# Kernel tuning notes

Hardware: AMD Instinct MI355X
Metric: run time of the kernel (lower is better)

## Reference

```python
import jax, jax.numpy as jnp
import numpy as np

EPS = 1e-06
K = 10
N, M, D, C = 65536, 1024, 2, 3


def setup_inputs() -> dict:
    key = jax.random.key(0)
    k1, k2, k3, k4 = jax.random.split(key, 4)
    x = jax.random.uniform(k1, (N, D), dtype=jnp.float32)            # query points (pixels)
    mus = jax.random.uniform(k2, (1, M, D), dtype=jnp.float32)        # gaussian means
    A = 0.1 * jax.random.normal(k3, (1, M, D, D), dtype=jnp.float32)  # random factor
    covs = A @ jnp.swapaxes(A, -1, -2) + 0.01 * jnp.eye(D, dtype=jnp.float32)  # SPD covariances
    cols = jax.random.uniform(k4, (1, M, C), dtype=jnp.float32)       # per-gaussian RGB
    return {"x": x, "mus": mus, "covs": covs, "cols": cols}


def reference(x, mus, covs, cols):
    # d: [N, M, D] point-to-mean offsets
    d = x[:, None, :] - mus[0]
    # solve covs @ s = d for each (point, gaussian) pair -> [N, M, D]
    s = jnp.linalg.solve(covs[0], d[..., None])[..., 0]
    # quadratic form d^T Sigma^{-1} d -> gaussian weights [N, M]
    gauss = jnp.exp(-0.5 * jnp.einsum('nmd,nmd->nm', d, s))
    k = min(K, mus.shape[1])
    vals, idx = jax.lax.top_k(gauss, k)              # [N, k]
    top_cols = cols[0][idx]                           # [N, k, C]
    raw = jnp.einsum('nk,nkc->nc', vals, top_cols)    # weighted color sum
    return raw / (vals.sum(-1, keepdims=True) + EPS)  # normalized [N, C]
```

## Files before the change

### kernel.cpp

```cpp
#include <hip/hip_runtime.h>
#include <stdint.h>

#define MG 1024
#define KTOP 10
#define EPSF 1e-6f
#define CXc 24
#define CYc 16
#define NCELL (CXc * CYc)
#define CAP 224
#define OVCAP 256
#define RHO 0.03757f
#define CSTRIDE 1040
#define CPAD 16
#define POISON 0xAAAAAAAAu

typedef unsigned long long u64;
typedef unsigned short u16;

__device__ __forceinline__ int cell_of(float x0, float x1) {
    int ix = (int)(x0 * CXc); ix = ix < 0 ? 0 : (ix > CXc - 1 ? CXc - 1 : ix);
    int iy = (int)(x1 * CYc); iy = iy < 0 ? 0 : (iy > CYc - 1 ? CYc - 1 : iy);
    return iy * CXc + ix;
}

__global__ __launch_bounds__(256) void k_prep(
    const float* __restrict__ x, const float* __restrict__ mus,
    const float* __restrict__ covs,
    uint32_t* __restrict__ counts, uint32_t* __restrict__ ovc,
    u16* __restrict__ ovlist, u16* __restrict__ buckets,
    float4* __restrict__ grec, float* __restrict__ grecC,
    u16* __restrict__ candM, uint32_t* __restrict__ ncand, int N)
{
    const int t = threadIdx.x, blk = blockIdx.x;
    if (blk < 256) {
        const int n = blk * 256 + t;
        if (n < MG) {
            const float4 cv = ((const float4*)covs)[n];
            const float2 mu = ((const float2*)mus)[n];
            const float inv = 1.0f / (cv.x * cv.w - cv.y * cv.z);
            grec[n]  = make_float4(mu.x, mu.y, -0.5f * cv.w * inv, cv.y * inv);
            grecC[n] = -0.5f * cv.x * inv;
        }
        if (n >= N) return;
        const float2 xv = ((const float2*)x)[n];
        const int c = cell_of(xv.x, xv.y);
        const uint32_t r = atomicAdd(&counts[c * CPAD], 1u) - POISON;
        if (r < CAP) buckets[c * CAP + r] = (u16)n;
        else { const uint32_t o = atomicAdd(ovc, 1u) - POISON; if (o < OVCAP) ovlist[o] = (u16)n; }
        return;
    }
    const int lane = t & 63;
    const int c = (blk - 256) * 4 + (t >> 6);
    const float cx = ((float)(c % CXc) + 0.5f) / (float)CXc;
    const float cy = ((float)(c / CXc) + 0.5f) / (float)CYc;
    const float INF = __builtin_huge_valf();

    float D10[KTOP], Uv[16];
    #pragma unroll
    for (int i = 0; i < KTOP; ++i) D10[i] = -INF;

    #pragma unroll
    for (int j = 0; j < 16; ++j) {
        const int m = j * 64 + lane;
        const float4 cv = ((const float4*)covs)[m];
        const float2 mu = ((const float2*)mus)[m];
        const float inv = 1.0f / (cv.x * cv.w - cv.y * cv.z);
        const float A = -0.5f * cv.w * inv, B = cv.y * inv, Cc = -0.5f * cv.x * inv;
        const float dx = cx - mu.x, dy = cy - mu.y;
        const float qc = fmaf(fmaf(A, dx, B * dy), dx, Cc * (dy * dy));
        const float S00 = -2.0f * A, S01 = -B, S11 = -2.0f * Cc;
        const float sx = S00 * dx + S01 * dy, sy = S01 * dx + S11 * dy;
        const float slack = sqrtf(fmaf(sx, sx, sy * sy)) * RHO;
        const float lr2 = 0.5f * (S00 + S11) * (RHO * RHO);
        const float eps = 1e-3f * (1.0f + fabsf(qc) + slack);
        Uv[j] = qc + slack + eps;
        const float D = qc - slack - lr2 - eps;
        bool cg[KTOP];
        #pragma unroll
        for (int i = 0; i < KTOP; ++i) cg[i] = D10[i] >= D;
        #pragma unroll
        for (int i = KTOP - 1; i >= 1; --i)
            D10[i] = cg[i] ? D10[i] : (cg[i - 1] ? D : D10[i - 1]);
        D10[0] = cg[0] ? D10[0] : D;
    }
    #pragma unroll
    for (int s = 1; s < 64; s <<= 1) {
        float ob[KTOP], na[KTOP];
        #pragma unroll
        for (int i = 0; i < KTOP; ++i) ob[i] = __shfl_xor(D10[i], s);
        #pragma unroll
        for (int i = 0; i < KTOP; ++i) {
            float best = -INF;
            #pragma unroll
            for (int j = 0; j <= i + 1 && j <= KTOP; ++j) {
                const int l = i + 1 - j;
                if (l > KTOP) continue;
                const float av = (j == 0) ? INF : D10[j - 1];
                const float bv = (l == 0) ? INF : ob[l - 1];
                best = fmaxf(best, fminf(av, bv));
            }
            na[i] = best;
        }
        #pragma unroll
        for (int i = 0; i < KTOP; ++i) D10[i] = na[i];
    }
    const float L = D10[KTOP - 1];

    const int base = c * CSTRIDE;
    const u64 below = (lane == 0) ? 0ull : ((~0ull) >> (64 - lane));
    int total = 0;
    #pragma unroll
    for (int j = 0; j < 16; ++j) {
        const bool keep = (Uv[j] >= L);
        const u64 bal = __ballot(keep);
        if (keep) {
            const int slot = total + (int)__popcll(bal & below);
            candM[base + slot] = (u16)(j * 64 + lane);
        }
        total += (int)__popcll(bal);
    }
    if (lane == 0) ncand[c] = (uint32_t)total;
}

__global__ __launch_bounds__(128) void k_main(
    const float* __restrict__ x, const float* __restrict__ cols,
    const float4* __restrict__ grec, const float* __restrict__ grecC,
    const uint32_t* __restrict__ counts, const uint32_t* __restrict__ ovc,
    const u16* __restrict__ ovlist, const u16* __restrict__ buckets,
    const u16* __restrict__ candM, const uint32_t* __restrict__ ncand,
    float* __restrict__ out, int N)
{
    __shared__ float4 l4[CSTRIDE];
    __shared__ __align__(16) float lC[CSTRIDE];
    __shared__ __align__(16) uint32_t lM[CSTRIDE];

    const int t = threadIdx.x;
    const int lane = t & 63, wv = t >> 6;
    const int b = blockIdx.x;

    u64 topk[KTOP];
    const u64 SENT = ((u64)0x007FFFFFull) << 10;
    #pragma unroll
    for (int j = 0; j < KTOP; ++j) topk[j] = SENT;
    float thr = __uint_as_float(0xff800000u);

    auto net_insert = [&](u64 key) {
        bool cg[KTOP];
        #pragma unroll
        for (int j = 0; j < KTOP; ++j) cg[j] = topk[j] >= key;
        #pragma unroll
        for (int j = KTOP - 1; j >= 1; --j)
            topk[j] = cg[j] ? topk[j] : (cg[j - 1] ? key : topk[j - 1]);
        topk[0] = cg[0] ? topk[0] : key;
    };
    auto ins = [&](float q, int m) {
        if (__any(q >= thr)) {
            const uint32_t bb = __float_as_uint(q);
            const uint32_t msk = (uint32_t)((int32_t)bb >> 31) | 0x80000000u;
            net_insert(((u64)(bb ^ msk) << 10) | (u64)(MG - 1 - m));
            const uint32_t kb = (uint32_t)(topk[KTOP - 1] >> 10);
            const uint32_t db = ((int32_t)kb < 0) ? (kb ^ 0x80000000u) : ~kb;
            thr = __uint_as_float(db);
        }
    };

    int pp = 0; bool valid = false;

    if (b >= 2 * NCELL) {
        const uint32_t oc = min(ovc[0] - POISON, (uint32_t)OVCAP);
        const uint32_t gi = (uint32_t)((b - 2 * NCELL) * 128 + t);
        if (oc == 0u || gi >= ((oc + 63u) & ~63u)) {
            if (__ballot(gi < oc) == 0ull) return;
        }
        int p = -1;
        if (gi < oc) p = (int)ovlist[gi];
        valid = (p >= 0);
        const int p0lane = __shfl(p, 0);
        pp = valid ? p : (p0lane >= 0 ? p0lane : 0);
        const float2 xv = ((const float2*)x)[pp];
        const float x0 = xv.x, x1 = xv.y;
        for (int m = 0; m < MG; m += 4) {
            const float4 g0 = grec[m], g1 = grec[m + 1], g2 = grec[m + 2], g3 = grec[m + 3];
            const float4 c4 = *(const float4*)&grecC[m];
            const float dx0 = x0 - g0.x, dy0 = x1 - g0.y;
            const float dx1 = x0 - g1.x, dy1 = x1 - g1.y;
            const float dx2 = x0 - g2.x, dy2 = x1 - g2.y;
            const float dx3 = x0 - g3.x, dy3 = x1 - g3.y;
            const float q0 = fmaf(fmaf(g0.z, dx0, g0.w * dy0), dx0, c4.x * (dy0 * dy0));
            const float q1 = fmaf(fmaf(g1.z, dx1, g1.w * dy1), dx1, c4.y * (dy1 * dy1));
            const float q2 = fmaf(fmaf(g2.z, dx2, g2.w * dy2), dx2, c4.z * (dy2 * dy2));
            const float q3 = fmaf(fmaf(g3.z, dx3, g3.w * dy3), dx3, c4.w * (dy3 * dy3));
            const float qm = fmaxf(fmaxf(q0, q1), fmaxf(q2, q3));
            if (__any(qm >= thr)) {
                ins(q0, m); ins(q1, m + 1); ins(q2, m + 2); ins(q3, m + 3);
            }
        }
    } else {
        const int c = b >> 1, h = b & 1;
        const int cnt = (int)min(counts[c * CPAD] - POISON, (uint32_t)CAP);
        if (h * 128 >= cnt) return;

        const int nc = (int)min(ncand[c], (uint32_t)(CSTRIDE - 4));
        const int ntot = (nc + 3) & ~3;
        const int cbase = c * CSTRIDE;
        for (int i = t; i < ntot; i += 128) {
            if (i < nc) {
                const int m = (int)candM[cbase + i];
                l4[i] = grec[m];
                lC[i] = grecC[m];
                lM[i] = (uint32_t)m;
            } else {
                l4[i] = make_float4(3e30f, 3e30f, -1.0f, 0.0f);
                lC[i] = -1.0f;
                lM[i] = 0u;
            }
        }
        __syncthreads();

        const int i = (h * 2 + wv) * 64 + lane;
        if ((h * 2 + wv) * 64 >= cnt) return;
        int p = -1;
        if (i < cnt) p = (int)buckets[c * CAP + i];
        valid = (p >= 0);
        const int p0lane = __shfl(p, 0);
        pp = valid ? p : p0lane;
        const float2 xv = ((const float2*)x)[pp];
        const float x0 = xv.x, x1 = xv.y;

        for (int i2 = 0; i2 < ntot; i2 += 4) {
            const float4 g0 = l4[i2], g1 = l4[i2 + 1], g2 = l4[i2 + 2], g3 = l4[i2 + 3];
            const float4 c4 = *(const float4*)&lC[i2];
            const uint4  m4 = *(const uint4*)&lM[i2];
            const float dx0 = x0 - g0.x, dy0 = x1 - g0.y;
            const float dx1 = x0 - g1.x, dy1 = x1 - g1.y;
            const float dx2 = x0 - g2.x, dy2 = x1 - g2.y;
            const float dx3 = x0 - g3.x, dy3 = x1 - g3.y;
            const float q0 = fmaf(fmaf(g0.z, dx0, g0.w * dy0), dx0, c4.x * (dy0 * dy0));
            const float q1 = fmaf(fmaf(g1.z, dx1, g1.w * dy1), dx1, c4.y * (dy1 * dy1));
            const float q2 = fmaf(fmaf(g2.z, dx2, g2.w * dy2), dx2, c4.z * (dy2 * dy2));
            const float q3 = fmaf(fmaf(g3.z, dx3, g3.w * dy3), dx3, c4.w * (dy3 * dy3));
            const float qm = fmaxf(fmaxf(q0, q1), fmaxf(q2, q3));
            if (__any(qm >= thr)) {
                ins(q0, (int)m4.x); ins(q1, (int)m4.y);
                ins(q2, (int)m4.z); ins(q3, (int)m4.w);
            }
        }
    }

    float vsum = 0.0f, rc = 0.0f, gc = 0.0f, bc = 0.0f;
    #pragma unroll
    for (int j = 0; j < KTOP; ++j) {
        const u64 key = topk[j];
        const int m = (MG - 1) - (int)(key & 1023u);
        const uint32_t kb = (uint32_t)(key >> 10);
        const uint32_t bb = ((int32_t)kb < 0) ? (kb ^ 0x80000000u) : ~kb;
        const float v = __expf(__uint_as_float(bb));
        vsum += v;
        rc = fmaf(v, cols[3 * m + 0], rc);
        gc = fmaf(v, cols[3 * m + 1], gc);
        bc = fmaf(v, cols[3 * m + 2], bc);
    }
    const float s = 1.0f / (vsum + EPSF);
    if (valid) {
        out[pp * 3 + 0] = rc * s;
        out[pp * 3 + 1] = gc * s;
        out[pp * 3 + 2] = bc * s;
    }
}

extern "C" void kernel_launch(void* const* d_in, const int* in_sizes, int n_in,
                              void* d_out, int out_size, void* d_ws, size_t ws_size,
                              hipStream_t stream) {
    const float* x    = (const float*)d_in[0];
    const float* mus  = (const float*)d_in[1];
    const float* covs = (const float*)d_in[2];
    const float* cols = (const float*)d_in[3];
    float* out = (float*)d_out;
    const int N = in_sizes[0] / 2;

    uint32_t* counts = (uint32_t*)d_ws;
    uint32_t* ovc    = counts + NCELL * CPAD;
    u16*      ovlist = (u16*)(ovc + 16);
    uintptr_t a = (uintptr_t)(ovlist + OVCAP);
    a = (a + 15) & ~(uintptr_t)15;
    float4*   grec   = (float4*)a;
    float*    grecC  = (float*)(grec + MG);
    u16*      buckets= (u16*)(grecC + MG);
    uint32_t* ncand  = (uint32_t*)(buckets + NCELL * CAP);
    u16*      candM  = (u16*)(ncand + NCELL);
    const size_t need = ((char*)(candM + NCELL * CSTRIDE)) - (char*)d_ws;

    if (ws_size >= need) {
        k_prep<<<256 + NCELL / 4, 256, 0, stream>>>(x, mus, covs, counts, ovc,
                                                    ovlist, buckets, grec, grecC,
                                                    candM, ncand, N);
        k_main<<<2 * NCELL + 2, 128, 0, stream>>>(x, cols, grec, grecC,
                                                  counts, ovc, ovlist, buckets,
                                                  candM, ncand, out, N);
    }
}
```

Before: 90.93 us.

## Bin points into finer sub-cells so each wave is spatially coherent

Points are now binned into a 96x32 sub-cell grid, and each coarse cell gathers its 8 sub-cells in order using a prefix sum. Each wavefront therefore holds points that sit close together, which should make the wave-level threshold tests in the top-k loop agree more often and skip more insertion work. The launch grows to three blocks per cell to cover the larger per-cell capacity. The cost is a larger counts array, a small prefix-sum search per lane, and extra blocks that mostly exit early.

```diff
diff --git a/kernel.cpp b/kernel.cpp
--- a/kernel.cpp
+++ b/kernel.cpp
@@ -7,7 +7,10 @@
 #define CXc 24
 #define CYc 16
 #define NCELL (CXc * CYc)
-#define CAP 224
+#define SCX 96
+#define SCY 32
+#define NSUB (SCX * SCY)
+#define CAPS 40
 #define OVCAP 256
 #define RHO 0.03757f
 #define CSTRIDE 1040
@@ -16,12 +19,6 @@
 
 typedef unsigned long long u64;
 typedef unsigned short u16;
-
-__device__ __forceinline__ int cell_of(float x0, float x1) {
-    int ix = (int)(x0 * CXc); ix = ix < 0 ? 0 : (ix > CXc - 1 ? CXc - 1 : ix);
-    int iy = (int)(x1 * CYc); iy = iy < 0 ? 0 : (iy > CYc - 1 ? CYc - 1 : iy);
-    return iy * CXc + ix;
-}
 
 __global__ __launch_bounds__(256) void k_prep(
     const float* __restrict__ x, const float* __restrict__ mus,
@@ -43,9 +40,11 @@
         }
         if (n >= N) return;
         const float2 xv = ((const float2*)x)[n];
-        const int c = cell_of(xv.x, xv.y);
-        const uint32_t r = atomicAdd(&counts[c * CPAD], 1u) - POISON;
-        if (r < CAP) buckets[c * CAP + r] = (u16)n;
+        int six = (int)(xv.x * SCX); six = six < 0 ? 0 : (six > SCX - 1 ? SCX - 1 : six);
+        int siy = (int)(xv.y * SCY); siy = siy < 0 ? 0 : (siy > SCY - 1 ? SCY - 1 : siy);
+        const int sub = siy * SCX + six;
+        const uint32_t r = atomicAdd(&counts[sub * CPAD], 1u) - POISON;
+        if (r < CAPS) buckets[sub * CAPS + r] = (u16)n;
         else { const uint32_t o = atomicAdd(ovc, 1u) - POISON; if (o < OVCAP) ovlist[o] = (u16)n; }
         return;
     }
@@ -166,12 +165,10 @@
 
     int pp = 0; bool valid = false;
 
-    if (b >= 2 * NCELL) {
+    if (b >= 3 * NCELL) {
         const uint32_t oc = min(ovc[0] - POISON, (uint32_t)OVCAP);
-        const uint32_t gi = (uint32_t)((b - 2 * NCELL) * 128 + t);
-        if (oc == 0u || gi >= ((oc + 63u) & ~63u)) {
-            if (__ballot(gi < oc) == 0ull) return;
-        }
+        const uint32_t gi = (uint32_t)((b - 3 * NCELL) * 128 + t);
+        if (__ballot(gi < oc) == 0ull) return;
         int p = -1;
         if (gi < oc) p = (int)ovlist[gi];
         valid = (p >= 0);
@@ -196,8 +193,18 @@
             }
         }
     } else {
-        const int c = b >> 1, h = b & 1;
-        const int cnt = (int)min(counts[c * CPAD] - POISON, (uint32_t)CAP);
+        const int c = b / 3, h = b % 3;
+        const int ccx = c % CXc, ccy = c / CXc;
+        int pre[9]; pre[0] = 0;
+        int subs[8];
+        #pragma unroll
+        for (int j = 0; j < 8; ++j) {
+            const int six = 4 * ccx + (j & 3), siy = 2 * ccy + (j >> 2);
+            subs[j] = siy * SCX + six;
+            const uint32_t cj = counts[subs[j] * CPAD] - POISON;
+            pre[j + 1] = pre[j] + (int)min(cj, (uint32_t)CAPS);
+        }
+        const int cnt = pre[8];
         if (h * 128 >= cnt) return;
 
         const int nc = (int)min(ncand[c], (uint32_t)(CSTRIDE - 4));
@@ -217,10 +224,15 @@
         }
         __syncthreads();
 
-        const int i = (h * 2 + wv) * 64 + lane;
+        const int slot = (h * 2 + wv) * 64 + lane;
         if ((h * 2 + wv) * 64 >= cnt) return;
         int p = -1;
-        if (i < cnt) p = (int)buckets[c * CAP + i];
+        if (slot < cnt) {
+            int j = 0;
+            #pragma unroll
+            for (int k = 1; k < 8; ++k) j += (slot >= pre[k]) ? 1 : 0;
+            p = (int)buckets[subs[j] * CAPS + (slot - pre[j])];
+        }
         valid = (p >= 0);
         const int p0lane = __shfl(p, 0);
         pp = valid ? p : p0lane;
@@ -279,14 +291,14 @@
     const int N = in_sizes[0] / 2;
 
     uint32_t* counts = (uint32_t*)d_ws;
-    uint32_t* ovc    = counts + NCELL * CPAD;
+    uint32_t* ovc    = counts + NSUB * CPAD;
     u16*      ovlist = (u16*)(ovc + 16);
     uintptr_t a = (uintptr_t)(ovlist + OVCAP);
     a = (a + 15) & ~(uintptr_t)15;
     float4*   grec   = (float4*)a;
     float*    grecC  = (float*)(grec + MG);
     u16*      buckets= (u16*)(grecC + MG);
-    uint32_t* ncand  = (uint32_t*)(buckets + NCELL * CAP);
+    uint32_t* ncand  = (uint32_t*)(buckets + NSUB * CAPS);
     u16*      candM  = (u16*)(ncand + NCELL);
     const size_t need = ((char*)(candM + NCELL * CSTRIDE)) - (char*)d_ws;
 
@@ -294,7 +306,7 @@
         k_prep<<<256 + NCELL / 4, 256, 0, stream>>>(x, mus, covs, counts, ovc,
                                                     ovlist, buckets, grec, grecC,
                                                     candM, ncand, N);
-        k_main<<<2 * NCELL + 2, 128, 0, stream>>>(x, cols, grec, grecC,
+        k_main<<<3 * NCELL + 2, 128, 0, stream>>>(x, cols, grec, grecC,
                                                   counts, ovc, ovlist, buckets,
                                                   candM, ncand, out, N);
     }
```

Result: no change. 91.70 us (+0.9%).
